# Performance work log

Measured on AMD Instinct MI355X. Metric: run time of the kernel, lower is better.

## Reference

```python
import jax, jax.numpy as jnp
import numpy as np

SR = 22050
L = 65537            # signal length; chosen so rfft length == L (required by source broadcast)
NFFT = 131072        # 2**ceil(log2(L))
RLEN = NFFT // 2 + 1 # == L
OUT_SIZE = 65537     # output_size init arg
BANDS = [("delta", 1.0, 4.0), ("theta", 4.0, 8.0), ("alpha", 8.0, 13.0),
         ("beta", 13.0, 30.0), ("gamma", 30.0, 100.0), ("high_gamma", 100.0, 200.0)]
SPEC = [("schumann", 7.83), ("healing", 528.0), ("solfeggio", 396.0), ("sleep", 2.5),
        ("focus", 14.1), ("harmony", 432.0), ("meditation", 6.0), ("energy", 30.0)]
FREQS_NP = np.fft.rfftfreq(NFFT, d=1.0 / SR).astype(np.float32)


def _prog_mean(hp, W1, b1, W2, b2, W3, b3):
    # vectorized get_harmonic_progression(arange(L)).mean()
    t = jnp.arange(L, dtype=jnp.float32)
    tn = (t / OUT_SIZE)[:, None]                       # [L,1]
    h = jax.nn.relu(tn @ W1 + b1)
    h = jax.nn.relu(h @ W2 + b2)
    mp = h @ W3 + b3                                   # [L,8]
    mod_depth = mp[0, 1]
    chord_idx = jnp.floor(t * 8.0 / OUT_SIZE).astype(jnp.int32) % 8
    chord = hp[chord_idx]                              # [L,4]
    chord = chord * (1.0 + mod_depth * jnp.sin(2.0 * jnp.pi * t / OUT_SIZE))[:, None]
    return chord.mean()


def _gain(bw, fw, hp, W1, b1, W2, b2, W3, b3):
    # all modulation is data-independent -> single [RLEN] multiplicative gain
    t = jnp.arange(L, dtype=jnp.float32)
    gain = jnp.ones(RLEN, dtype=jnp.float32)
    for k, (_, low, high) in enumerate(BANDS):
        center = (low + high) / 2.0
        width = (high - low) / 2.0
        m_np = np.exp(-0.5 * ((FREQS_NP - center) / (width / 2.0)) ** 2)
        m_np[(FREQS_NP < low) | (FREQS_NP > high)] = 0.0
        if not np.any(m_np > 0.01):  # static branch (mask is data-independent)
            continue
        mask = jnp.asarray(m_np.astype(np.float32))     # [RLEN] == [L]
        time_mod = jnp.sin(2.0 * jnp.pi * center * t / SR)
        gain = gain * (1.0 + mask * bw[k] * (1.0 + 0.2 * time_mod))
    pm = _prog_mean(hp, W1, b1, W2, b2, W3, b3)
    ws = min(15, NFFT // 100)
    ws = ws if ws > 0 else 1
    for j, (_, f) in enumerate(SPEC):
        if f >= SR / 2:
            continue
        for mult in (1.0, 2.0, 3.0, 4.0, 5.0):
            hf = f * mult
            if hf >= SR / 2:
                continue
            hidx = int(np.argmin(np.abs(FREQS_NP - hf)))
            s = max(0, hidx - ws)
            e = min(RLEN - 1, hidx + ws)
            if s >= e:
                continue
            idxs = np.arange(s, e + 1)
            win = jnp.asarray(np.exp(-0.5 * ((idxs - hidx) / (ws / 3.0)) ** 2).astype(np.float32))
            enh = fw[j] * win * (1.0 / mult ** 1.2) * (1.0 + pm)
            gain = gain.at[s:e + 1].multiply(1.0 + enh)
    return gain


def _forward(x, bw, fw, hp, W1, b1, W2, b2, W3, b3):
    gain = _gain(bw, fw, hp, W1, b1, W2, b2, W3, b3)    # [RLEN]
    xp = jnp.pad(x, ((0, 0), (0, 0), (0, NFFT - L)))    # zero-pad to n_fft
    X = jnp.fft.rfft(xp, axis=-1) * gain                # [B,C,RLEN] complex
    mag = jnp.abs(X)
    ph = jnp.angle(X)
    mid = 0.7 * mag[..., 1:-1] + 0.15 * mag[..., :-2] + 0.15 * mag[..., 2:]
    mag_s = jnp.concatenate([mag[..., :1], mid, mag[..., -1:]], axis=-1)
    Xc = mag_s * jnp.exp(1j * ph)
    y = jnp.fft.irfft(Xc, n=NFFT, axis=-1)[..., :L]
    return y.astype(x.dtype)


def setup_inputs() -> dict:
    key = jax.random.key(0)
    ks = jax.random.split(key, 8)
    B, C = 128, 2
    x = jax.random.normal(ks[0], (B, C, L), dtype=jnp.float32)
    band_weights = jnp.full((6,), 0.5, dtype=jnp.float32)
    freq_weights = jnp.full((8,), 0.3, dtype=jnp.float32)
    harmonic_progression = jax.random.normal(ks[1], (8, 4), dtype=jnp.float32)
    W1 = jax.random.normal(ks[2], (1, 32), dtype=jnp.float32)
    b1 = jnp.zeros((32,), dtype=jnp.float32)
    W2 = jax.random.normal(ks[3], (32, 16), dtype=jnp.float32) * (1.0 / np.sqrt(32.0))
    b2 = jnp.zeros((16,), dtype=jnp.float32)
    W3 = jax.random.normal(ks[4], (16, 8), dtype=jnp.float32) * (1.0 / np.sqrt(16.0))
    b3 = jnp.zeros((8,), dtype=jnp.float32)
    return {"x": x, "band_weights": band_weights, "freq_weights": freq_weights,
            "harmonic_progression": harmonic_progression,
            "W1": W1, "b1": b1, "W2": W2, "b2": b2, "W3": W3, "b3": b3}


def reference(x, band_weights, freq_weights, harmonic_progression, W1, b1, W2, b2, W3, b3):
    return _forward(x, band_weights, freq_weights, harmonic_progression, W1, b1, W2, b2, W3, b3)
```

## Files before the change

### kernel.cpp

```cpp
#include <hip/hip_runtime.h>
#include <hip/hip_fp16.h>
#include <math.h>

#define L_SIG 65537
#define NH    65536
#define NSIG  256
#define PI_F  3.14159265358979323846f

struct alignas(8) c32 { float x, y; };
typedef __half2 h2;
__device__ __forceinline__ c32 mkc(float a, float b){ c32 r; r.x=a; r.y=b; return r; }
__device__ __forceinline__ c32 cadd(c32 a, c32 b){ return mkc(a.x+b.x, a.y+b.y); }
__device__ __forceinline__ c32 csub(c32 a, c32 b){ return mkc(a.x-b.x, a.y-b.y); }
__device__ __forceinline__ c32 cmul(c32 a, c32 b){ return mkc(a.x*b.x - a.y*b.y, a.x*b.y + a.y*b.x); }
__device__ __forceinline__ h2  c2h(c32 a){ return __floats2half2_rn(a.x, a.y); }
__device__ __forceinline__ c32 h2c(h2 a){ float2 f = __half22float2(a); return mkc(f.x, f.y); }

template<int S>
__device__ __forceinline__ void fft16(c32 v[16]) {
  constexpr float C16[16] = {
    1.0f, 0.9238795325112867f, 0.7071067811865476f, 0.3826834323650898f,
    0.0f,-0.3826834323650898f,-0.7071067811865476f,-0.9238795325112867f,
   -1.0f,-0.9238795325112867f,-0.7071067811865476f,-0.3826834323650898f,
    0.0f, 0.3826834323650898f, 0.7071067811865476f, 0.9238795325112867f };
  constexpr float S16[16] = {
    0.0f, 0.3826834323650898f, 0.7071067811865476f, 0.9238795325112867f,
    1.0f, 0.9238795325112867f, 0.7071067811865476f, 0.3826834323650898f,
    0.0f,-0.3826834323650898f,-0.7071067811865476f,-0.9238795325112867f,
   -1.0f,-0.9238795325112867f,-0.7071067811865476f,-0.3826834323650898f };
  c32 s[16];
  #pragma unroll
  for (int b0 = 0; b0 < 4; ++b0) {
    c32 x0=v[b0], x1=v[b0+4], x2=v[b0+8], x3=v[b0+12];
    c32 u0=cadd(x0,x2), u1=csub(x0,x2), u2=cadd(x1,x3), u3=csub(x1,x3);
    c32 iu3 = mkc(-u3.y, u3.x);
    c32 yy[4];
    yy[0]=cadd(u0,u2); yy[2]=csub(u0,u2);
    if (S < 0) { yy[1]=csub(u1,iu3); yy[3]=cadd(u1,iu3); }
    else       { yy[1]=cadd(u1,iu3); yy[3]=csub(u1,iu3); }
    #pragma unroll
    for (int c0 = 0; c0 < 4; ++c0) {
      const int p = (b0*c0) & 15;
      c32 w = mkc(C16[p], (S<0) ? -S16[p] : S16[p]);
      s[c0*4 + b0] = cmul(yy[c0], w);
    }
  }
  #pragma unroll
  for (int c0 = 0; c0 < 4; ++c0) {
    c32 x0=s[c0*4+0], x1=s[c0*4+1], x2=s[c0*4+2], x3=s[c0*4+3];
    c32 u0=cadd(x0,x2), u1=csub(x0,x2), u2=cadd(x1,x3), u3=csub(x1,x3);
    c32 iu3 = mkc(-u3.y, u3.x);
    c32 yy[4];
    yy[0]=cadd(u0,u2); yy[2]=csub(u0,u2);
    if (S < 0) { yy[1]=csub(u1,iu3); yy[3]=cadd(u1,iu3); }
    else       { yy[1]=cadd(u1,iu3); yy[3]=csub(u1,iu3); }
    v[c0+0]=yy[0]; v[c0+4]=yy[1]; v[c0+8]=yy[2]; v[c0+12]=yy[3];
  }
}

template<int S>
__device__ __forceinline__ void fft256_team(c32 v[16], int r, int t, c32* sc) {
  fft16<S>(v);
  float ang = (float)S * (2.0f*PI_F/256.0f) * (float)r;
  c32 st; __sincosf(ang, &st.y, &st.x);
  c32 w = st;
  #pragma unroll
  for (int c = 1; c < 16; ++c) { v[c] = cmul(v[c], w); w = cmul(w, st); }
  int p  = r*8 + (t & 7);
  int fr = (r & 1) << 3;
  __syncthreads();
  if (t < 8) {
    #pragma unroll
    for (int c = 0; c < 16; ++c)
      sc[c*128 + (p ^ ((c & 1) << 3))] = v[c];
  }
  __syncthreads();
  if (t < 8) {
    #pragma unroll
    for (int a = 0; a < 16; ++a)
      v[a] = sc[r*128 + ((a*8 + (t & 7)) ^ fr)];
  }
  __syncthreads();
  if (t >= 8) {
    #pragma unroll
    for (int c = 0; c < 16; ++c)
      sc[c*128 + (p ^ ((c & 1) << 3))] = v[c];
  }
  __syncthreads();
  if (t >= 8) {
    #pragma unroll
    for (int a = 0; a < 16; ++a)
      v[a] = sc[r*128 + ((a*8 + (t & 7)) ^ fr)];
  }
  fft16<S>(v);
}

__global__ __launch_bounds__(256) void k_pm(const float* __restrict__ hp,
                                            float* __restrict__ pm_part) {
  __shared__ float r0[256], r1[256];
  int t = threadIdx.x, b = blockIdx.x;
  int gid = b*256 + t;
  float s0 = 0.f, s1 = 0.f;
  for (int tt = gid; tt < 65537; tt += 16384) {
    int ci = (tt * 8) / 65537;
    float cs = hp[ci*4+0] + hp[ci*4+1] + hp[ci*4+2] + hp[ci*4+3];
    float ang = (6.2831853071795864769f * (float)tt) / 65537.0f;
    s0 += cs;
    s1 += cs * sinf(ang);
  }
  r0[t] = s0; r1[t] = s1;
  __syncthreads();
  for (int s = 128; s > 0; s >>= 1) {
    if (t < s) { r0[t] += r0[t+s]; r1[t] += r1[t+s]; }
    __syncthreads();
  }
  if (t == 0) { pm_part[2*b] = r0[0]; pm_part[2*b+1] = r1[0]; }
}

__global__ __launch_bounds__(256) void k_prep2(const float* __restrict__ b1,
    const float* __restrict__ W2, const float* __restrict__ b2,
    const float* __restrict__ W3, const float* __restrict__ b3,
    const float* __restrict__ fw, const float* __restrict__ pm_part,
    float* __restrict__ pm_out, int* __restrict__ hidx, float* __restrict__ amp) {
  __shared__ float r0[64], r1[64];
  __shared__ float s_pm;
  int t = threadIdx.x;
  if (t < 64) { r0[t] = pm_part[2*t]; r1[t] = pm_part[2*t+1]; }
  __syncthreads();
  if (t == 0) {
    float h1[32], h2v[16];
    for (int i=0;i<32;i++){ float z = b1[i]; h1[i] = z > 0.f ? z : 0.f; }
    for (int o=0;o<16;o++){ float acc = b2[o];
      for (int i=0;i<32;i++) acc += h1[i]*W2[i*16+o];
      h2v[o] = acc > 0.f ? acc : 0.f; }
    float md = b3[1];
    for (int i=0;i<16;i++) md += h2v[i]*W3[i*8+1];
    float S0 = 0.f, S1 = 0.f;
    for (int i=0;i<64;i++){ S0 += r0[i]; S1 += r1[i]; }
    s_pm = (S0 + md*S1) / (65537.0f * 4.0f);
    pm_out[0] = s_pm;
  }
  __syncthreads();
  if (t < 40) {
    const double SPECF[8] = {7.83, 528.0, 396.0, 2.5, 14.1, 432.0, 6.0, 30.0};
    int j = t / 5, mi = t % 5;
    double mult = (double)(mi + 1);
    double hf = SPECF[j] * mult;
    double ratio = hf * (131072.0 / 22050.0);
    hidx[t] = (int)floor(ratio + 0.5);
    amp[t] = (float)((double)fw[j] * pow(mult, -1.2) * (1.0 + (double)s_pm));
  }
}

__global__ __launch_bounds__(256) void k_gain(float* __restrict__ gainT,
    const float* __restrict__ bw, const int* __restrict__ hidx,
    const float* __restrict__ amp) {
  int j = blockIdx.x*256 + threadIdx.x;
  if (j > 65536) return;
  int i = (j == 65536) ? 65536 : (((j >> 8) & 255) | ((j & 255) << 8));
  float f = (float)((double)i * (22050.0/131072.0));
  float g = 1.0f;
  constexpr double LO[6] = {1,4,8,13,30,100};
  constexpr double HI[6] = {4,8,13,30,100,200};
  #pragma unroll
  for (int k = 0; k < 6; ++k) {
    float center = (float)(0.5*(LO[k]+HI[k]));
    float sig    = (float)(0.25*(HI[k]-LO[k]));
    float dm = (f - center)/sig;
    float mask = expf(-0.5f*dm*dm);
    if (f < (float)LO[k] || f > (float)HI[k]) mask = 0.f;
    float ang = (float)(6.283185307179586*0.5*(LO[k]+HI[k])) * (float)i / 22050.0f;
    g *= 1.0f + mask * bw[k] * (1.0f + 0.2f*sinf(ang));
  }
  for (int l = 0; l < 40; ++l) {
    int d = i - hidx[l];
    if (d >= -15 && d <= 15) {
      float dd = (float)d * 0.2f;
      g *= 1.0f + amp[l] * expf(-0.5f*dd*dd);
    }
  }
  gainT[j] = g;
}

__global__ __launch_bounds__(256, 4) void k_fwd1(const float* __restrict__ x,
                                                 h2* __restrict__ A, int s0) {
  __shared__ float smem[4096];
  c32* sc = (c32*)smem;
  h2*  stg = (h2*)smem;
  int b = blockIdx.x; int sl = b >> 4; int g = b & 15;
  int t = threadIdx.x & 15, r = threadIdx.x >> 4;
  int n1 = g*16 + t;
  const float* xb = x + (size_t)(s0 + sl) * L_SIG;
  c32 v[16];
  #pragma unroll
  for (int j = 0; j < 16; ++j) {
    int n = n1 + 256*r + 4096*j;
    c32 z = mkc(0.f, 0.f);
    if (n < 32768)       { z.x = xb[2*n]; z.y = xb[2*n+1]; }
    else if (n == 32768) { z.x = xb[65536]; }
    v[j] = z;
  }
  fft256_team<-1>(v, r, t, sc);
  float a0 = -(2.0f*PI_F/65536.0f) * (float)(n1 * r);
  float a1 = -(2.0f*PI_F/4096.0f)  * (float)n1;
  c32 wb, wst;
  __sincosf(a0, &wb.y, &wb.x);
  __sincosf(a1, &wst.y, &wst.x);
  #pragma unroll
  for (int j = 0; j < 16; ++j) { v[j] = cmul(v[j], wb); wb = cmul(wb, wst); }
  __syncthreads();
  #pragma unroll
  for (int j = 0; j < 16; ++j)
    stg[(r + 16*j)*16 + t] = c2h(v[j]);
  __syncthreads();
  h2* Ab = A + (size_t)sl * NH;
  int u = threadIdx.x & 15, k2b = threadIdx.x >> 4;
  #pragma unroll
  for (int m = 0; m < 16; ++m) {
    int k2 = k2b + 16*m;
    Ab[(size_t)k2*256 + g*16 + u] = stg[k2*16 + u];
  }
}

__global__ __launch_bounds__(256, 4) void k_fwd2(const h2* __restrict__ A,
                                                 h2* __restrict__ ZT) {
  __shared__ float smem[4160];
  c32* sc = (c32*)smem;
  h2* stg = (h2*)smem;
  int b = blockIdx.x; int sl = b >> 4; int g = b & 15;
  int tid = threadIdx.x;
  int t = tid & 15, r = tid >> 4;
  const h2* Ab = A + (size_t)sl * NH;
  #pragma unroll
  for (int m = 0; m < 4; ++m) {
    int flat = tid + 256*m;
    int row = flat >> 6, i = flat & 63;
    float4 z = ((const float4*)(Ab + (size_t)(g*16 + row)*256))[i];
    *((float4*)&stg[row*260 + 4*i]) = z;
  }
  __syncthreads();
  c32 v[16];
  #pragma unroll
  for (int j = 0; j < 16; ++j)
    v[j] = h2c(stg[t*260 + r + 16*j]);
  fft256_team<-1>(v, r, t, sc);
  __syncthreads();
  #pragma unroll
  for (int j = 0; j < 16; ++j)
    stg[t*260 + r + 16*j] = c2h(v[j]);
  __syncthreads();
  h2* Zb = ZT + (size_t)sl * NH;
  #pragma unroll
  for (int w = 0; w < 4; ++w) {
    int flat = tid + 256*w;
    int k2l = flat >> 6, i = flat & 63;
    *((float4*)(Zb + (size_t)(g*16 + k2l)*256 + 4*i)) =
        *((const float4*)(stg + k2l*260 + 4*i));
  }
}

struct UP { c32 Uk, UK; float mk, mK, cn, sn; };
__device__ __forceinline__ UP pairupG(const h2* __restrict__ Zs, int k,
                                      const float* __restrict__ gT) {
  UP u;
  int kk = k & (NH-1);
  int Km = (NH - k) & (NH-1);
  int ik = ((kk & 255) << 8) | (kk >> 8);
  int ib = ((Km & 255) << 8) | (Km >> 8);
  c32 zk = h2c(Zs[ik]);
  c32 zb = h2c(Zs[ib]);
  c32 Aa = mkc(0.5f*(zk.x + zb.x), 0.5f*(zk.y - zb.y));
  c32 Bm = mkc(0.5f*(zk.x - zb.x), 0.5f*(zk.y + zb.y));
  __sincosf((PI_F/65536.0f)*(float)k, &u.sn, &u.cn);
  c32 wB = cmul(mkc(-u.sn, -u.cn), Bm);
  float gk = gT[ik];
  int K2 = NH - k;
  float gK = (K2 >= NH) ? gT[NH] : gT[ib];
  c32 Xk = mkc((Aa.x + wB.x)*gk,  (Aa.y + wB.y)*gk);
  c32 XK = mkc((Aa.x - wB.x)*gK, -(Aa.y - wB.y)*gK);
  float nk = Xk.x*Xk.x + Xk.y*Xk.y;
  float nK = XK.x*XK.x + XK.y*XK.y;
  float rk = rsqrtf(nk), rK = rsqrtf(nK);
  bool kv = (k >= 0);
  u.Uk = (nk > 0.f) ? mkc(Xk.x*rk, Xk.y*rk) : mkc(1.f, 0.f);
  u.UK = (nK > 0.f) ? mkc(XK.x*rK, XK.y*rK) : mkc(1.f, 0.f);
  u.mk = (kv && nk > 0.f) ? nk*rk : 0.f;
  u.mK = (kv && nK > 0.f) ? nK*rK : 0.f;
  return u;
}

__global__ __launch_bounds__(256, 4) void k_mi(const h2* __restrict__ ZT,
                                               h2* __restrict__ B,
                                               const float* __restrict__ gT) {
  __shared__ float smem[4420];
  h2*  rowsO = (h2*)smem;
  c32* sc    = (c32*)smem;
  h2*  stg   = (h2*)smem;
  int b = blockIdx.x; int sl = b >> 4; int p = b & 15;
  int tid = threadIdx.x; int t = tid & 15; int r = tid >> 4;
  const h2* Zs = ZT + (size_t)sl * NH;
  h2* Bb = B + (size_t)sl * NH;
  int m = tid;
  int K0 = 8*p - 1 + 256*m;
  h2 o1[8], o2[8]; h2 o128 = __floats2half2_rn(0.f, 0.f);
  float m1a=0.f, m1b=0.f, m2a=0.f, m2b=0.f, cnp=0.f, snp=0.f;
  c32 u1p = mkc(1.f,0.f), u2p = mkc(1.f,0.f);
  const float invN = 1.0f/65536.0f;
  #pragma unroll
  for (int s = 0; s <= 9; ++s) {
    UP u = pairupG(Zs, K0 + s, gT);
    if (s >= 2) {
      int kq = K0 + s - 1;
      float msm = (kq == 0) ? m1b : 0.7f*m1b + 0.15f*(m1a + u.mk);
      float msh = (kq == 0) ? m2b : 0.7f*m2b + 0.15f*(m2a + u.mK);
      c32 XcL = mkc(u1p.x*msm, u1p.y*msm);
      c32 XcH = mkc(u2p.x*msh, u2p.y*msh);
      c32 E = mkc(0.5f*(XcL.x + XcH.x), 0.5f*(XcL.y - XcH.y));
      c32 D = mkc(0.5f*(XcL.x - XcH.x), 0.5f*(XcL.y + XcH.y));
      c32 O = cmul(mkc(cnp, snp), D);
      o1[s-2] = c2h(mkc((E.x - O.y)*invN, (E.y + O.x)*invN));
      o2[s-2] = c2h(mkc((E.x + O.y)*invN, (O.x - E.y)*invN));
    }
    m1a = m1b; m1b = u.mk; m2a = m2b; m2b = u.mK;
    u1p = u.Uk; u2p = u.UK; cnp = u.cn; snp = u.sn;
  }
  if (p == 15) {
    int kb = 128 + 256*m;
    UP uA = pairupG(Zs, kb - 1, gT);
    UP u8 = pairupG(Zs, kb,     gT);
    UP uB = pairupG(Zs, kb + 1, gT);
    float msm = 0.7f*u8.mk + 0.15f*(uA.mk + uB.mk);
    float msh = 0.7f*u8.mK + 0.15f*(uA.mK + uB.mK);
    c32 XcL = mkc(u8.Uk.x*msm, u8.Uk.y*msm);
    c32 XcH = mkc(u8.UK.x*msh, u8.UK.y*msh);
    c32 E = mkc(0.5f*(XcL.x + XcH.x), 0.5f*(XcL.y - XcH.y));
    c32 D = mkc(0.5f*(XcL.x - XcH.x), 0.5f*(XcL.y + XcH.y));
    c32 O = cmul(mkc(u8.cn, u8.sn), D);
    o128 = c2h(mkc((E.x - O.y)*invN, (E.y + O.x)*invN));
  }
  #pragma unroll
  for (int s = 1; s <= 8; ++s) {
    rowsO[(s-1)*260 + m] = o1[s-1];
    int kq = K0 + s;
    if (kq != 0) {
      int Kq = (NH - kq) & (NH-1);
      rowsO[(16 - s)*260 + (Kq >> 8)] = o2[s-1];
    }
  }
  if (p == 15) rowsO[16*260 + m] = o128;
  __syncthreads();
  {
    int aT = (t < 8) ? (8*p + t) : (249 - 8*p + (t - 8));
    c32 v[16];
    #pragma unroll
    for (int j = 0; j < 16; ++j) v[j] = h2c(rowsO[t*260 + r + 16*j]);
    fft256_team<1>(v, r, t, sc);
    float a0 = (2.0f*PI_F/65536.0f) * (float)(aT * r);
    float a1 = (2.0f*PI_F/4096.0f)  * (float)aT;
    c32 wb, wst;
    __sincosf(a0, &wb.y, &wb.x);
    __sincosf(a1, &wst.y, &wst.x);
    #pragma unroll
    for (int j = 0; j < 16; ++j) { v[j] = cmul(v[j], wb); wb = cmul(wb, wst); }
    __syncthreads();
    #pragma unroll
    for (int j = 0; j < 16; ++j) stg[(r + 16*j)*16 + t] = c2h(v[j]);
    __syncthreads();
    int u = tid & 15, mb = tid >> 4;
    int aU = (u < 8) ? (8*p + u) : (249 - 8*p + (u - 8));
    if (aU < 256) {
      #pragma unroll
      for (int q = 0; q < 16; ++q) {
        int m2 = mb + 16*q;
        Bb[(size_t)m2*256 + aU] = stg[m2*16 + u];
      }
    }
  }
  if (p == 15) {
    c32 v[16];
    #pragma unroll
    for (int j = 0; j < 16; ++j) v[j] = h2c(rowsO[16*260 + r + 16*j]);
    fft256_team<1>(v, r, t, sc);
    float a0 = (2.0f*PI_F/65536.0f) * (float)(128 * r);
    float a1 = (2.0f*PI_F/4096.0f)  * 128.0f;
    c32 wb, wst;
    __sincosf(a0, &wb.y, &wb.x);
    __sincosf(a1, &wst.y, &wst.x);
    #pragma unroll
    for (int j = 0; j < 16; ++j) { v[j] = cmul(v[j], wb); wb = cmul(wb, wst); }
    __syncthreads();
    #pragma unroll
    for (int j = 0; j < 16; ++j) stg[(r + 16*j)*16 + t] = c2h(v[j]);
    __syncthreads();
    int u = tid & 15, mb = tid >> 4;
    if (u == 0) {
      #pragma unroll
      for (int q = 0; q < 16; ++q) {
        int m2 = mb + 16*q;
        Bb[(size_t)m2*256 + 128] = stg[m2*16 + 0];
      }
    }
  }
}

__global__ __launch_bounds__(256, 4) void k_inv2(const h2* __restrict__ B,
                                                 float* __restrict__ out, int s0) {
  __shared__ float smem[4160];
  c32* sc = (c32*)smem;
  h2* stg = (h2*)smem;
  int b = blockIdx.x; int sl = b >> 4; int g = b & 15;
  int tid = threadIdx.x;
  int t = tid & 15, r = tid >> 4;
  const h2* Bb = B + (size_t)sl * NH;
  #pragma unroll
  for (int m = 0; m < 4; ++m) {
    int flat = tid + 256*m;
    int row = flat >> 6, i = flat & 63;
    float4 z = ((const float4*)(Bb + (size_t)(g*16 + row)*256))[i];
    *((float4*)&stg[row*260 + 4*i]) = z;
  }
  __syncthreads();
  c32 v[16];
  #pragma unroll
  for (int j = 0; j < 16; ++j)
    v[j] = h2c(stg[t*260 + r + 16*j]);
  fft256_team<1>(v, r, t, sc);
  float* yb = out + (size_t)(s0 + sl) * L_SIG;
  int m2 = g*16 + t;
  #pragma unroll
  for (int j = 0; j < 16; ++j) {
    int m1 = r + 16*j;
    if (m1 <= 127) {
      int m = m2 + 256*m1;
      yb[2*m]   = v[j].x;
      yb[2*m+1] = v[j].y;
    } else if (m1 == 128 && m2 == 0) {
      yb[65536] = v[j].x;
    }
  }
}

extern "C" void kernel_launch(void* const* d_in, const int* in_sizes, int n_in,
                              void* d_out, int out_size, void* d_ws, size_t ws_size,
                              hipStream_t stream) {
  const float* x  = (const float*)d_in[0];
  const float* bw = (const float*)d_in[1];
  const float* fw = (const float*)d_in[2];
  const float* hp = (const float*)d_in[3];
  const float* b1 = (const float*)d_in[5];
  const float* W2 = (const float*)d_in[6];
  const float* b2 = (const float*)d_in[7];
  const float* W3 = (const float*)d_in[8];
  const float* b3 = (const float*)d_in[9];
  float* out = (float*)d_out;
  char* ws = (char*)d_ws;

  const size_t perSig = (size_t)NH * sizeof(h2);
  const size_t tail   = (size_t)L_SIG * sizeof(float) + 2048;
  size_t cap = (ws_size > tail) ? (ws_size - tail) / (2*perSig) : 1;
  int chunk = (cap >= (size_t)NSIG) ? NSIG : (cap < 1 ? 1 : (int)cap);

  h2*    A     = (h2*)ws;
  h2*    Bb    = (h2*)(ws + (size_t)chunk*perSig);
  float* gainT = (float*)(ws + 2*(size_t)chunk*perSig);
  float* pm    = gainT + L_SIG;
  int*   hidx  = (int*)(pm + 1);
  float* amp   = (float*)(hidx + 40);
  float* pm_part = amp + 40;

  k_pm   <<<64, 256, 0, stream>>>(hp, pm_part);
  k_prep2<<<1,  256, 0, stream>>>(b1, W2, b2, W3, b3, fw, pm_part, pm, hidx, amp);
  k_gain <<<257,256, 0, stream>>>(gainT, bw, hidx, amp);

  for (int s0 = 0; s0 < NSIG; s0 += chunk) {
    int S = (NSIG - s0 < chunk) ? (NSIG - s0) : chunk;
    k_fwd1<<<S*16, 256, 0, stream>>>(x, A, s0);
    k_fwd2<<<S*16, 256, 0, stream>>>(A, Bb);
    k_mi  <<<S*16, 256, 0, stream>>>(Bb, A, gainT);
    k_inv2<<<S*16, 256, 0, stream>>>(A, out, s0);
  }
}
```

Before: 325.3 us.

## Drop conjugate-pair reuse in k_mi; compute 16 contiguous columns per block

```diff
diff --git a/kernel.cpp b/kernel.cpp
--- a/kernel.cpp
+++ b/kernel.cpp
@@ -273,7 +273,7 @@
   c32 Bm = mkc(0.5f*(zk.x - zb.x), 0.5f*(zk.y + zb.y));
   __sincosf((PI_F/65536.0f)*(float)k, &u.sn, &u.cn);
   c32 wB = cmul(mkc(-u.sn, -u.cn), Bm);
-  float gk = gT[ik];
+  float gk = (k >= NH) ? gT[NH] : gT[ik];
   int K2 = NH - k;
   float gK = (K2 >= NH) ? gT[NH] : gT[ib];
   c32 Xk = mkc((Aa.x + wB.x)*gk,  (Aa.y + wB.y)*gk);
@@ -292,22 +292,22 @@
 __global__ __launch_bounds__(256, 4) void k_mi(const h2* __restrict__ ZT,
                                                h2* __restrict__ B,
                                                const float* __restrict__ gT) {
-  __shared__ float smem[4420];
+  __shared__ float smem[4160];
   h2*  rowsO = (h2*)smem;
   c32* sc    = (c32*)smem;
   h2*  stg   = (h2*)smem;
-  int b = blockIdx.x; int sl = b >> 4; int p = b & 15;
+  int b = blockIdx.x; int sl = b >> 4; int g = b & 15;
   int tid = threadIdx.x; int t = tid & 15; int r = tid >> 4;
   const h2* Zs = ZT + (size_t)sl * NH;
   h2* Bb = B + (size_t)sl * NH;
   int m = tid;
-  int K0 = 8*p - 1 + 256*m;
-  h2 o1[8], o2[8]; h2 o128 = __floats2half2_rn(0.f, 0.f);
+  int K0 = 16*g - 1 + 256*m;
+  h2 o1[16];
   float m1a=0.f, m1b=0.f, m2a=0.f, m2b=0.f, cnp=0.f, snp=0.f;
   c32 u1p = mkc(1.f,0.f), u2p = mkc(1.f,0.f);
   const float invN = 1.0f/65536.0f;
   #pragma unroll
-  for (int s = 0; s <= 9; ++s) {
+  for (int s = 0; s <= 17; ++s) {
     UP u = pairupG(Zs, K0 + s, gT);
     if (s >= 2) {
       int kq = K0 + s - 1;
@@ -319,87 +319,36 @@
       c32 D = mkc(0.5f*(XcL.x - XcH.x), 0.5f*(XcL.y + XcH.y));
       c32 O = cmul(mkc(cnp, snp), D);
       o1[s-2] = c2h(mkc((E.x - O.y)*invN, (E.y + O.x)*invN));
-      o2[s-2] = c2h(mkc((E.x + O.y)*invN, (O.x - E.y)*invN));
     }
     m1a = m1b; m1b = u.mk; m2a = m2b; m2b = u.mK;
     u1p = u.Uk; u2p = u.UK; cnp = u.cn; snp = u.sn;
   }
-  if (p == 15) {
-    int kb = 128 + 256*m;
-    UP uA = pairupG(Zs, kb - 1, gT);
-    UP u8 = pairupG(Zs, kb,     gT);
-    UP uB = pairupG(Zs, kb + 1, gT);
-    float msm = 0.7f*u8.mk + 0.15f*(uA.mk + uB.mk);
-    float msh = 0.7f*u8.mK + 0.15f*(uA.mK + uB.mK);
-    c32 XcL = mkc(u8.Uk.x*msm, u8.Uk.y*msm);
-    c32 XcH = mkc(u8.UK.x*msh, u8.UK.y*msh);
-    c32 E = mkc(0.5f*(XcL.x + XcH.x), 0.5f*(XcL.y - XcH.y));
-    c32 D = mkc(0.5f*(XcL.x - XcH.x), 0.5f*(XcL.y + XcH.y));
-    c32 O = cmul(mkc(u8.cn, u8.sn), D);
-    o128 = c2h(mkc((E.x - O.y)*invN, (E.y + O.x)*invN));
-  }
-  #pragma unroll
-  for (int s = 1; s <= 8; ++s) {
-    rowsO[(s-1)*260 + m] = o1[s-1];
-    int kq = K0 + s;
-    if (kq != 0) {
-      int Kq = (NH - kq) & (NH-1);
-      rowsO[(16 - s)*260 + (Kq >> 8)] = o2[s-1];
-    }
-  }
-  if (p == 15) rowsO[16*260 + m] = o128;
-  __syncthreads();
-  {
-    int aT = (t < 8) ? (8*p + t) : (249 - 8*p + (t - 8));
-    c32 v[16];
-    #pragma unroll
-    for (int j = 0; j < 16; ++j) v[j] = h2c(rowsO[t*260 + r + 16*j]);
-    fft256_team<1>(v, r, t, sc);
-    float a0 = (2.0f*PI_F/65536.0f) * (float)(aT * r);
-    float a1 = (2.0f*PI_F/4096.0f)  * (float)aT;
-    c32 wb, wst;
-    __sincosf(a0, &wb.y, &wb.x);
-    __sincosf(a1, &wst.y, &wst.x);
-    #pragma unroll
-    for (int j = 0; j < 16; ++j) { v[j] = cmul(v[j], wb); wb = cmul(wb, wst); }
-    __syncthreads();
-    #pragma unroll
-    for (int j = 0; j < 16; ++j) stg[(r + 16*j)*16 + t] = c2h(v[j]);
-    __syncthreads();
-    int u = tid & 15, mb = tid >> 4;
-    int aU = (u < 8) ? (8*p + u) : (249 - 8*p + (u - 8));
-    if (aU < 256) {
-      #pragma unroll
-      for (int q = 0; q < 16; ++q) {
-        int m2 = mb + 16*q;
-        Bb[(size_t)m2*256 + aU] = stg[m2*16 + u];
-      }
-    }
-  }
-  if (p == 15) {
-    c32 v[16];
-    #pragma unroll
-    for (int j = 0; j < 16; ++j) v[j] = h2c(rowsO[16*260 + r + 16*j]);
-    fft256_team<1>(v, r, t, sc);
-    float a0 = (2.0f*PI_F/65536.0f) * (float)(128 * r);
-    float a1 = (2.0f*PI_F/4096.0f)  * 128.0f;
-    c32 wb, wst;
-    __sincosf(a0, &wb.y, &wb.x);
-    __sincosf(a1, &wst.y, &wst.x);
-    #pragma unroll
-    for (int j = 0; j < 16; ++j) { v[j] = cmul(v[j], wb); wb = cmul(wb, wst); }
-    __syncthreads();
-    #pragma unroll
-    for (int j = 0; j < 16; ++j) stg[(r + 16*j)*16 + t] = c2h(v[j]);
-    __syncthreads();
-    int u = tid & 15, mb = tid >> 4;
-    if (u == 0) {
-      #pragma unroll
-      for (int q = 0; q < 16; ++q) {
-        int m2 = mb + 16*q;
-        Bb[(size_t)m2*256 + 128] = stg[m2*16 + 0];
-      }
-    }
+  #pragma unroll
+  for (int s = 0; s < 16; ++s)
+    rowsO[s*260 + m] = o1[s];
+  __syncthreads();
+  int a = g*16 + t;
+  c32 v[16];
+  #pragma unroll
+  for (int j = 0; j < 16; ++j) v[j] = h2c(rowsO[t*260 + r + 16*j]);
+  fft256_team<1>(v, r, t, sc);
+  float a0 = (2.0f*PI_F/65536.0f) * (float)(a * r);
+  float a1 = (2.0f*PI_F/4096.0f)  * (float)a;
+  c32 wb, wst;
+  __sincosf(a0, &wb.y, &wb.x);
+  __sincosf(a1, &wst.y, &wst.x);
+  #pragma unroll
+  for (int j = 0; j < 16; ++j) { v[j] = cmul(v[j], wb); wb = cmul(wb, wst); }
+  __syncthreads();
+  #pragma unroll
+  for (int j = 0; j < 16; ++j)
+    stg[(r + 16*j)*16 + t] = c2h(v[j]);
+  __syncthreads();
+  int u = tid & 15, m2b_ = tid >> 4;
+  #pragma unroll
+  for (int q = 0; q < 16; ++q) {
+    int m2 = m2b_ + 16*q;
+    Bb[(size_t)m2*256 + g*16 + u] = stg[m2*16 + u];
   }
 }
 
```

Result: faster. 290.7 us (-10.6%).
